# Kernel tuning notes

Hardware: AMD Instinct MI355X
Metric: run time of the kernel (lower is better)

## Reference

```python
import jax, jax.numpy as jnp
import numpy as np

B, S, H, D = 2, 2048, 16, 128
HID = H * D
THETA = 10000.0
SCALE = 1.0 / np.sqrt(D)


def setup_inputs() -> dict:
    key = jax.random.key(0)
    k1, k2, k3 = jax.random.split(key, 3)
    x = jax.random.normal(k1, (B, S, HID), dtype=jnp.float32)
    w_qkv = jax.random.normal(k2, (3 * HID, HID), dtype=jnp.float32) * 0.02
    w_o = jax.random.normal(k3, (HID, HID), dtype=jnp.float32) * 0.02
    return {"x": x, "w_qkv": w_qkv, "w_o": w_o}


def _rope_cos_sin(seq_len, dim, dtype):
    inv_freq = 1.0 / (THETA ** (jnp.arange(0, dim, 2, dtype=jnp.float32) / dim))
    pos = jnp.arange(seq_len, dtype=jnp.float32)
    freqs = pos[:, None] * inv_freq[None, :]          # (S, D/2)
    emb = jnp.concatenate([freqs, freqs], axis=-1)    # (S, D)
    return jnp.cos(emb).astype(dtype), jnp.sin(emb).astype(dtype)


def _rotate_half(t):
    t1, t2 = jnp.split(t, 2, axis=-1)
    return jnp.concatenate([-t2, t1], axis=-1)


def reference(x, w_qkv, w_o):
    b, s, _ = x.shape
    qkv = jnp.einsum('bsh,oh->bso', x, w_qkv)                 # (B,S,3*HID)
    qkv = qkv.reshape(b, s, 3, H, D).transpose(2, 0, 3, 1, 4)  # (3,B,H,S,D)
    q, k, v = qkv[0], qkv[1], qkv[2]
    cos, sin = _rope_cos_sin(s, D, x.dtype)                    # (S,D)
    q = q * cos + _rotate_half(q) * sin
    k = k * cos + _rotate_half(k) * sin
    scores = jnp.einsum('bhqd,bhkd->bhqk', q, k) * SCALE       # (B,H,S,S)
    causal = jnp.triu(jnp.ones((s, s), dtype=bool), k=1)
    scores = jnp.where(causal[None, None], -jnp.inf, scores)
    attn = jax.nn.softmax(scores.astype(jnp.float32), axis=-1).astype(q.dtype)
    out = jnp.einsum('bhqk,bhkd->bhqd', attn, v)               # (B,H,S,D)
    out = out.transpose(0, 2, 1, 3).reshape(b, s, HID)
    return jnp.einsum('bsh,oh->bso', out, w_o)
```

## Files before the change

kernel.cpp:

```cpp
#include <hip/hip_runtime.h>
#include <hip/hip_bf16.h>

typedef unsigned short u16;
typedef unsigned long long u64;
typedef u16 us8 __attribute__((ext_vector_type(8)));
typedef __bf16 bf8_t __attribute__((ext_vector_type(8)));
typedef float f32x4 __attribute__((ext_vector_type(4)));

__device__ __forceinline__ float b2f(u16 u) {
    return __uint_as_float(((unsigned int)u) << 16);
}
__device__ __forceinline__ u16 f2b(float f) {
    union { __hip_bfloat16 h; u16 u; } v;
    v.h = __float2bfloat16(f);
    return v.u;
}
__device__ __forceinline__ f32x4 mfma16(bf8_t a, bf8_t b, f32x4 c) {
    return __builtin_amdgcn_mfma_f32_16x16x32_bf16(a, b, c, 0, 0, 0);
}
__device__ __forceinline__ void gload_lds16(const u16* g, u16* lds_base) {
    __builtin_amdgcn_global_load_lds((const __attribute__((address_space(1))) unsigned int*)g,
                                     (__attribute__((address_space(3))) unsigned int*)lds_base,
                                     16, 0, 0);
}

__global__ __launch_bounds__(256) void f32_to_bf16(const float* __restrict__ src,
                                                   u16* __restrict__ dst, int n8) {
    int idx = blockIdx.x * 256 + threadIdx.x;
    if (idx >= n8) return;
    float4 f0 = ((const float4*)src)[idx * 2];
    float4 f1 = ((const float4*)src)[idx * 2 + 1];
    us8 o;
    o[0] = f2b(f0.x); o[1] = f2b(f0.y); o[2] = f2b(f0.z); o[3] = f2b(f0.w);
    o[4] = f2b(f1.x); o[5] = f2b(f1.y); o[6] = f2b(f1.z); o[7] = f2b(f1.w);
    ((us8*)dst)[idx] = o;
}

#define BARX() __builtin_amdgcn_s_barrier()
#define LGKM0() do { asm volatile("s_waitcnt lgkmcnt(0)" ::: "memory"); \
                     __builtin_amdgcn_sched_barrier(0); } while (0)
#define VM4()   do { asm volatile("s_waitcnt vmcnt(4)" ::: "memory"); \
                     __builtin_amdgcn_sched_barrier(0); } while (0)

template<int SF32>
__global__ __launch_bounds__(512, 2) void gemm256(const u16* __restrict__ A,
                                                  const u16* __restrict__ B,
                                                  void* __restrict__ Cout, int ldc) {
    __shared__ u16 LA[2][256 * 64];
    __shared__ u16 LB[2][256 * 64];

    const int tid = threadIdx.x;
    const int w = tid >> 6, lane = tid & 63;
    const int lm = lane & 15, lq = lane >> 4;
    const int wm = w >> 2, wn = w & 3;

    const int bid = blockIdx.x;
    const int nper = gridDim.x >> 3;
    const int wg = (bid & 7) * nper + (bid >> 3);
    const int mt = wg & 15, nt = wg >> 4;
    const int m0 = mt * 256, n0 = nt * 256;

    const int lp = lane ^ ((lane & 32) >> 4);
    const int srow = lp >> 3;
    const int scol = (lp & 7) * 8;

    const u16* Ag = A + (size_t)(m0 + srow) * 2048 + scol;
    const u16* Bg = B + (size_t)(n0 + srow) * 2048 + scol;

#define STAGE_A(c, h, kt) do { \
    _Pragma("unroll") \
    for (int i = 0; i < 2; i++) { \
        int R = w * 2 + i; \
        gload_lds16(Ag + (size_t)((h) * 128 + R * 8) * 2048 + (kt) * 64, \
                    &LA[c][((h) * 128 + R * 8) * 64]); \
    } } while (0)

#define STAGE_B(c, h, kt) do { \
    _Pragma("unroll") \
    for (int i = 0; i < 2; i++) { \
        int R = w * 2 + i; \
        gload_lds16(Bg + (size_t)((h) * 128 + R * 8) * 2048 + (kt) * 64, \
                    &LB[c][((h) * 128 + R * 8) * 64]); \
    } } while (0)

    bf8_t af[8][2], bfr[4][2];
    f32x4 acc[8][4] = {};

#define RD_A(c, mh) do { \
    _Pragma("unroll") \
    for (int m = 0; m < 4; m++) \
    _Pragma("unroll") \
    for (int ks = 0; ks < 2; ks++) { \
        int o = (wm * 128 + ((mh) * 4 + m) * 16 + lm) * 128 + ks * 64 + lq * 16; \
        o ^= ((o >> 9) & 1) << 5; \
        af[(mh) * 4 + m][ks] = *(const bf8_t*)((const char*)&LA[c][0] + o); \
    } } while (0)

#define RD_B(c, nh) do { \
    _Pragma("unroll") \
    for (int n = 0; n < 2; n++) \
    _Pragma("unroll") \
    for (int ks = 0; ks < 2; ks++) { \
        int o = (wn * 64 + ((nh) * 2 + n) * 16 + lm) * 128 + ks * 64 + lq * 16; \
        o ^= ((o >> 9) & 1) << 5; \
        bfr[(nh) * 2 + n][ks] = *(const bf8_t*)((const char*)&LB[c][0] + o); \
    } } while (0)

#define QUAD(mh, nh) do { \
    __builtin_amdgcn_s_setprio(1); \
    _Pragma("unroll") \
    for (int m = 0; m < 4; m++) \
    _Pragma("unroll") \
    for (int n = 0; n < 2; n++) \
    _Pragma("unroll") \
    for (int ks = 0; ks < 2; ks++) \
        acc[(mh) * 4 + m][(nh) * 2 + n] = mfma16(af[(mh) * 4 + m][ks], \
            bfr[(nh) * 2 + n][ks], acc[(mh) * 4 + m][(nh) * 2 + n]); \
    __builtin_amdgcn_s_setprio(0); \
    } while (0)

#define TILE(c, tB, tA) do { \
    RD_A(c, 0); RD_B(c, 0); \
    STAGE_B((c) ^ 1, 0, tB); \
    BARX(); LGKM0(); \
    QUAD(0, 0); \
    BARX(); \
    RD_A(c, 1); \
    STAGE_B((c) ^ 1, 1, tB); \
    BARX(); LGKM0(); \
    QUAD(1, 0); \
    BARX(); \
    RD_B(c, 1); \
    STAGE_A(c, 0, tA); \
    BARX(); LGKM0(); \
    QUAD(0, 1); \
    BARX(); \
    STAGE_A(c, 1, tA); \
    QUAD(1, 1); \
    VM4(); \
    BARX(); \
} while (0)

    STAGE_A(0, 0, 0); STAGE_A(0, 1, 0);
    STAGE_B(0, 0, 0); STAGE_B(0, 1, 0);
    STAGE_A(1, 0, 1); STAGE_A(1, 1, 1);
    VM4();
    BARX();

    for (int it = 0; it < 16; it++) {
        const int t0 = 2 * it, t1 = 2 * it + 1;
        const int tB0 = t1;
        const int tA0 = (t0 + 2 < 32) ? t0 + 2 : 31;
        const int tB1 = (t1 + 1 < 32) ? t1 + 1 : 31;
        const int tA1 = (t1 + 2 < 32) ? t1 + 2 : 31;
        TILE(0, tB0, tA0);
        TILE(1, tB1, tA1);
    }

#pragma unroll
    for (int m = 0; m < 8; m++)
#pragma unroll
        for (int n = 0; n < 4; n++)
#pragma unroll
            for (int r = 0; r < 4; r++) {
                int row = m0 + wm * 128 + m * 16 + lq * 4 + r;
                int col = n0 + wn * 64 + n * 16 + lm;
                if (SF32)
                    ((float*)Cout)[(size_t)row * ldc + col] = acc[m][n][r];
                else
                    ((u16*)Cout)[(size_t)row * ldc + col] = f2b(acc[m][n][r]);
            }
#undef TILE
#undef QUAD
#undef RD_A
#undef RD_B
#undef STAGE_A
#undef STAGE_B
}

__global__ __launch_bounds__(256) void rope_vt(u16* __restrict__ qkv, u16* __restrict__ VT) {
    __shared__ u16 T[64 * 136];
    const int tid = threadIdx.x;
    const int s0 = blockIdx.x * 64;
    const int bh = blockIdx.y;
    const int b = bh >> 4, h = bh & 15;
#pragma unroll
    for (int p = 0; p < 4; p++) {
        int sl = p * 16 + (tid >> 4);
        int d0 = (tid & 15) * 8;
        *(us8*)&T[sl * 136 + d0] =
            *(const us8*)(qkv + ((size_t)(b * 2048 + s0 + sl)) * 6144 + 4096 + h * 128 + d0);
    }
#pragma unroll
    for (int p = 0; p < 2; p++) {
        int task = p * 256 + tid;
        int sl = task >> 3;
        int jg = task & 7;
        size_t base = ((size_t)(b * 2048 + s0 + sl)) * 6144 + h * 128 + jg * 8;
        us8 qlo = *(const us8*)(qkv + base);
        us8 qhi = *(const us8*)(qkv + base + 64);
        us8 klo = *(const us8*)(qkv + base + 2048);
        us8 khi = *(const us8*)(qkv + base + 2048 + 64);
        us8 oql, oqh, okl, okh;
        float s = (float)(s0 + sl);
#pragma unroll
        for (int e = 0; e < 8; e++) {
            int j = jg * 8 + e;
            float inv = __expf((float)j * (-9.210340371976184f / 64.f));
            float ang = s * inv;
            float sn, c;
            __sincosf(ang, &sn, &c);
            float q1 = b2f(qlo[e]), q2 = b2f(qhi[e]);
            oql[e] = f2b(q1 * c - q2 * sn);
            oqh[e] = f2b(q2 * c + q1 * sn);
            float k1 = b2f(klo[e]), k2 = b2f(khi[e]);
            okl[e] = f2b(k1 * c - k2 * sn);
            okh[e] = f2b(k2 * c + k1 * sn);
        }
        *(us8*)(qkv + base) = oql;
        *(us8*)(qkv + base + 64) = oqh;
        *(us8*)(qkv + base + 2048) = okl;
        *(us8*)(qkv + base + 2048 + 64) = okh;
    }
    __syncthreads();
#pragma unroll
    for (int p = 0; p < 4; p++) {
        int idx = p * 256 + tid;
        int d = idx & 127;
        int sg = idx >> 7;
        us8 v;
#pragma unroll
        for (int i = 0; i < 8; i++) v[i] = T[(sg * 8 + i) * 136 + d];
        *(us8*)&VT[((size_t)bh * 128 + d) * 2048 + s0 + sg * 8] = v;
    }
}

#define ATT_SCALE 0.08838834764831845f

__global__ __launch_bounds__(256, 2) void attn_flash(const u16* __restrict__ qkv, const u16* __restrict__ VT,
                                                     u16* __restrict__ AO) {
    const int bid = blockIdx.x;
    const int swz = (bid & 7) * 64 + (bid >> 3);
    const int bh = swz >> 4;
    const int pair = swz & 15;
    const int b = bh >> 4, h = bh & 15;
    const int tid = threadIdx.x, lane = tid & 63, wave = tid >> 6;
    const int lm = lane & 15, lq = lane >> 4;

    const int jq0 = 31 - pair;
    const int jq1 = pair;
    const int ktmax = jq0;

    __shared__ u16 Kt[64 * 136];
    __shared__ u16 Vt[128 * 72];

    bf8_t qf[2][4];
#pragma unroll
    for (int qg = 0; qg < 2; qg++) {
        const int jqv = qg ? jq1 : jq0;
        const u16* Qrow = qkv + ((size_t)(b * 2048 + jqv * 64 + wave * 16 + lm)) * 6144 + h * 128;
#pragma unroll
        for (int ks = 0; ks < 4; ks++)
            qf[qg][ks] = *(const bf8_t*)(Qrow + ks * 32 + lq * 8);
    }

    f32x4 Of[2][8] = {};
    float mrun[2] = {-3.0e38f, -3.0e38f}, lrun[2] = {0.f, 0.f};

    const u16* Kbase = qkv + (size_t)b * 2048 * 6144 + 2048 + h * 128;
    const u16* VTbase = VT + (size_t)bh * 128 * 2048;

    const int krow = tid >> 4;
    const int kcol = (tid & 15) * 8;
    const int vrow = tid >> 3;
    const int vcol = (tid & 7) * 8;

    us8 kreg[4], vreg[4];
#pragma unroll
    for (int p = 0; p < 4; p++) {
        kreg[p] = *(const us8*)(Kbase + (size_t)(p * 16 + krow) * 6144 + kcol);
        vreg[p] = *(const us8*)(VTbase + (size_t)(p * 32 + vrow) * 2048 + vcol);
    }

    for (int kt = 0; kt <= ktmax; kt++) {
        __syncthreads();
#pragma unroll
        for (int p = 0; p < 4; p++) {
            *(us8*)&Kt[(p * 16 + krow) * 136 + kcol] = kreg[p];
            *(us8*)&Vt[(p * 32 + vrow) * 72 + vcol] = vreg[p];
        }
        __syncthreads();
        {
            int kn = (kt + 1 <= ktmax ? kt + 1 : ktmax) * 64;
#pragma unroll
            for (int p = 0; p < 4; p++) {
                kreg[p] = *(const us8*)(Kbase + (size_t)(kn + p * 16 + krow) * 6144 + kcol);
                vreg[p] = *(const us8*)(VTbase + (size_t)(p * 32 + vrow) * 2048 + kn + vcol);
            }
        }

        const bool act1 = (kt <= jq1);
        u64 pk[2][4];
#pragma unroll
        for (int qg = 0; qg < 2; qg++) {
            if (qg == 0 || act1) {
                const int jqv = qg ? jq1 : jq0;
                float sv[4][4];
#pragma unroll
                for (int nb = 0; nb < 4; nb++) {
                    f32x4 a = {};
#pragma unroll
                    for (int ks = 0; ks < 4; ks++) {
                        bf8_t kf = *(const bf8_t*)&Kt[(nb * 16 + lm) * 136 + ks * 32 + lq * 8];
                        a = mfma16(kf, qf[qg][ks], a);
                    }
#pragma unroll
                    for (int r = 0; r < 4; r++) sv[nb][r] = a[r] * ATT_SCALE;
                }
                if (kt == jqv) {
                    int qglob = jqv * 64 + wave * 16 + lm;
#pragma unroll
                    for (int nb = 0; nb < 4; nb++)
#pragma unroll
                        for (int r = 0; r < 4; r++)
                            if (kt * 64 + nb * 16 + lq * 4 + r > qglob) sv[nb][r] = -3.0e38f;
                }
                float mx = -3.0e38f;
#pragma unroll
                for (int nb = 0; nb < 4; nb++)
#pragma unroll
                    for (int r = 0; r < 4; r++) mx = fmaxf(mx, sv[nb][r]);
                mx = fmaxf(mx, __shfl_xor(mx, 16, 64));
                mx = fmaxf(mx, __shfl_xor(mx, 32, 64));
                float mnew = fmaxf(mrun[qg], mx);
                float a_ = __expf(mrun[qg] - mnew);
                float rs = 0.f;
#pragma unroll
                for (int nb = 0; nb < 4; nb++) {
                    float e0 = __expf(sv[nb][0] - mnew), e1 = __expf(sv[nb][1] - mnew);
                    float e2 = __expf(sv[nb][2] - mnew), e3 = __expf(sv[nb][3] - mnew);
                    rs += (e0 + e1) + (e2 + e3);
                    unsigned int lo = (unsigned int)f2b(e0) | ((unsigned int)f2b(e1) << 16);
                    unsigned int hi = (unsigned int)f2b(e2) | ((unsigned int)f2b(e3) << 16);
                    pk[qg][nb] = (u64)lo | ((u64)hi << 32);
                }
                rs += __shfl_xor(rs, 16, 64);
                rs += __shfl_xor(rs, 32, 64);
                lrun[qg] = lrun[qg] * a_ + rs;
                mrun[qg] = mnew;
#pragma unroll
                for (int db = 0; db < 8; db++)
#pragma unroll
                    for (int r = 0; r < 4; r++) Of[qg][db][r] *= a_;
            }
        }

        const int slo = ((lq & 1) * 2) * 16 + lm;
        const int shi = slo + 16;
        const bool sel = (lq >> 1) != 0;
#pragma unroll
        for (int kk = 0; kk < 2; kk++) {
            union { u64 v[2]; bf8_t f; } pf[2];
#pragma unroll
            for (int qg = 0; qg < 2; qg++) {
                if (qg == 0 || act1) {
                    u64 lo0 = __shfl(pk[qg][2 * kk + 0], slo, 64);
                    u64 lo1 = __shfl(pk[qg][2 * kk + 1], slo, 64);
                    u64 hi0 = __shfl(pk[qg][2 * kk + 0], shi, 64);
                    u64 hi1 = __shfl(pk[qg][2 * kk + 1], shi, 64);
                    pf[qg].v[0] = sel ? lo1 : lo0;
                    pf[qg].v[1] = sel ? hi1 : hi0;
                }
            }
#pragma unroll
            for (int db = 0; db < 8; db++) {
                bf8_t vf = *(const bf8_t*)&Vt[(db * 16 + lm) * 72 + kk * 32 + lq * 8];
                Of[0][db] = mfma16(vf, pf[0].f, Of[0][db]);
                if (act1) Of[1][db] = mfma16(vf, pf[1].f, Of[1][db]);
            }
        }
    }
#pragma unroll
    for (int qg = 0; qg < 2; qg++) {
        const int jqv = qg ? jq1 : jq0;
        float invl = 1.f / lrun[qg];
        size_t rowbase = (size_t)(b * 2048 + jqv * 64 + wave * 16 + lm) * 2048 + h * 128;
#pragma unroll
        for (int db = 0; db < 8; db++) {
            ushort4 o;
            o.x = f2b(Of[qg][db][0] * invl);
            o.y = f2b(Of[qg][db][1] * invl);
            o.z = f2b(Of[qg][db][2] * invl);
            o.w = f2b(Of[qg][db][3] * invl);
            *(ushort4*)(AO + rowbase + db * 16 + lq * 4) = o;
        }
    }
}

extern "C" void kernel_launch(void* const* d_in, const int* in_sizes, int n_in,
                              void* d_out, int out_size, void* d_ws, size_t ws_size,
                              hipStream_t stream) {
    const float* x     = (const float*)d_in[0];
    const float* w_qkv = (const float*)d_in[1];
    const float* w_o   = (const float*)d_in[2];
    float* out = (float*)d_out;
    u16* ws = (u16*)d_ws;

    u16* qkvb  = ws;
    u16* VT    = ws + 25165824;
    u16* AO    = ws + 33554432;
    u16* xb    = ws + 41943040;
    u16* wqkvb = ws + 50331648;
    u16* wob   = ws + 62914560;

    f32_to_bf16<<<4096, 256, 0, stream>>>(x, xb, 1048576);
    f32_to_bf16<<<6144, 256, 0, stream>>>(w_qkv, wqkvb, 1572864);
    f32_to_bf16<<<2048, 256, 0, stream>>>(w_o, wob, 524288);
    gemm256<0><<<384, 512, 0, stream>>>(xb, wqkvb, qkvb, 6144);
    rope_vt<<<dim3(32, 32), 256, 0, stream>>>(qkvb, VT);
    attn_flash<<<dim3(512), 256, 0, stream>>>(qkvb, VT, AO);
    gemm256<1><<<128, 512, 0, stream>>>(AO, wob, out, 2048);
}
```

Measured before the change: 454.2 us.

## Template GEMM on M-tile height; use 128-row tiles for output projection

Adds an AH template parameter so the GEMM can use 128x256 tiles instead of 256x256. The output projection now launches 256 workgroups instead of 128, which fills more of the CUs on the chip. The LDS swizzle also changes from a single-bit XOR to a full 8-way XOR of column chunks by row, to cut bank conflicts on fragment reads. Smaller tiles reuse each loaded operand less, and the changed swizzle now applies to the QKV GEMM as well.

```diff
diff --git a/kernel.cpp b/kernel.cpp
--- a/kernel.cpp
+++ b/kernel.cpp
@@ -39,14 +39,19 @@
 #define BARX() __builtin_amdgcn_s_barrier()
 #define LGKM0() do { asm volatile("s_waitcnt lgkmcnt(0)" ::: "memory"); \
                      __builtin_amdgcn_sched_barrier(0); } while (0)
-#define VM4()   do { asm volatile("s_waitcnt vmcnt(4)" ::: "memory"); \
-                     __builtin_amdgcn_sched_barrier(0); } while (0)
-
-template<int SF32>
+#define VMN() do { \
+    if constexpr (AH == 2) asm volatile("s_waitcnt vmcnt(4)" ::: "memory"); \
+    else                   asm volatile("s_waitcnt vmcnt(2)" ::: "memory"); \
+    __builtin_amdgcn_sched_barrier(0); } while (0)
+
+template<int SF32, int AH>
 __global__ __launch_bounds__(512, 2) void gemm256(const u16* __restrict__ A,
                                                   const u16* __restrict__ B,
                                                   void* __restrict__ Cout, int ldc) {
-    __shared__ u16 LA[2][256 * 64];
+    constexpr int MF = AH * 4;
+    constexpr int MH = AH * 2;
+
+    __shared__ u16 LA[2][AH * 128 * 64];
     __shared__ u16 LB[2][256 * 64];
 
     const int tid = threadIdx.x;
@@ -57,12 +62,12 @@
     const int bid = blockIdx.x;
     const int nper = gridDim.x >> 3;
     const int wg = (bid & 7) * nper + (bid >> 3);
-    const int mt = wg & 15, nt = wg >> 4;
-    const int m0 = mt * 256, n0 = nt * 256;
-
-    const int lp = lane ^ ((lane & 32) >> 4);
-    const int srow = lp >> 3;
-    const int scol = (lp & 7) * 8;
+    const int mt = (AH == 2) ? (wg & 15) : (wg & 31);
+    const int nt = (AH == 2) ? (wg >> 4) : (wg >> 5);
+    const int m0 = mt * (AH * 128), n0 = nt * 256;
+
+    const int srow = lane >> 3;
+    const int scol = ((lane & 7) ^ srow) * 8;
 
     const u16* Ag = A + (size_t)(m0 + srow) * 2048 + scol;
     const u16* Bg = B + (size_t)(n0 + srow) * 2048 + scol;
@@ -83,17 +88,18 @@
                     &LB[c][((h) * 128 + R * 8) * 64]); \
     } } while (0)
 
-    bf8_t af[8][2], bfr[4][2];
-    f32x4 acc[8][4] = {};
+    bf8_t af[MF][2], bfr[4][2];
+    f32x4 acc[MF][4] = {};
+    const int cswz = (lm & 7) << 4;
 
 #define RD_A(c, mh) do { \
     _Pragma("unroll") \
-    for (int m = 0; m < 4; m++) \
+    for (int m = 0; m < MH; m++) \
     _Pragma("unroll") \
     for (int ks = 0; ks < 2; ks++) { \
-        int o = (wm * 128 + ((mh) * 4 + m) * 16 + lm) * 128 + ks * 64 + lq * 16; \
-        o ^= ((o >> 9) & 1) << 5; \
-        af[(mh) * 4 + m][ks] = *(const bf8_t*)((const char*)&LA[c][0] + o); \
+        int row = wm * (AH * 64) + ((mh) * MH + m) * 16 + lm; \
+        int o = (row * 128 + ks * 64 + lq * 16) ^ cswz; \
+        af[(mh) * MH + m][ks] = *(const bf8_t*)((const char*)&LA[c][0] + o); \
     } } while (0)
 
 #define RD_B(c, nh) do { \
@@ -101,21 +107,21 @@
     for (int n = 0; n < 2; n++) \
     _Pragma("unroll") \
     for (int ks = 0; ks < 2; ks++) { \
-        int o = (wn * 64 + ((nh) * 2 + n) * 16 + lm) * 128 + ks * 64 + lq * 16; \
-        o ^= ((o >> 9) & 1) << 5; \
+        int row = wn * 64 + ((nh) * 2 + n) * 16 + lm; \
+        int o = (row * 128 + ks * 64 + lq * 16) ^ cswz; \
         bfr[(nh) * 2 + n][ks] = *(const bf8_t*)((const char*)&LB[c][0] + o); \
     } } while (0)
 
 #define QUAD(mh, nh) do { \
     __builtin_amdgcn_s_setprio(1); \
     _Pragma("unroll") \
-    for (int m = 0; m < 4; m++) \
+    for (int m = 0; m < MH; m++) \
     _Pragma("unroll") \
     for (int n = 0; n < 2; n++) \
     _Pragma("unroll") \
     for (int ks = 0; ks < 2; ks++) \
-        acc[(mh) * 4 + m][(nh) * 2 + n] = mfma16(af[(mh) * 4 + m][ks], \
-            bfr[(nh) * 2 + n][ks], acc[(mh) * 4 + m][(nh) * 2 + n]); \
+        acc[(mh) * MH + m][(nh) * 2 + n] = mfma16(af[(mh) * MH + m][ks], \
+            bfr[(nh) * 2 + n][ks], acc[(mh) * MH + m][(nh) * 2 + n]); \
     __builtin_amdgcn_s_setprio(0); \
     } while (0)
 
@@ -135,16 +141,18 @@
     BARX(); LGKM0(); \
     QUAD(0, 1); \
     BARX(); \
-    STAGE_A(c, 1, tA); \
+    if constexpr (AH == 2) STAGE_A(c, 1, tA); \
     QUAD(1, 1); \
-    VM4(); \
+    VMN(); \
     BARX(); \
 } while (0)
 
-    STAGE_A(0, 0, 0); STAGE_A(0, 1, 0);
+    STAGE_A(0, 0, 0);
+    if constexpr (AH == 2) STAGE_A(0, 1, 0);
     STAGE_B(0, 0, 0); STAGE_B(0, 1, 0);
-    STAGE_A(1, 0, 1); STAGE_A(1, 1, 1);
-    VM4();
+    STAGE_A(1, 0, 1);
+    if constexpr (AH == 2) STAGE_A(1, 1, 1);
+    VMN();
     BARX();
 
     for (int it = 0; it < 16; it++) {
@@ -158,12 +166,12 @@
     }
 
 #pragma unroll
-    for (int m = 0; m < 8; m++)
+    for (int m = 0; m < MF; m++)
 #pragma unroll
         for (int n = 0; n < 4; n++)
 #pragma unroll
             for (int r = 0; r < 4; r++) {
-                int row = m0 + wm * 128 + m * 16 + lq * 4 + r;
+                int row = m0 + wm * (AH * 64) + m * 16 + lq * 4 + r;
                 int col = n0 + wn * 64 + n * 16 + lm;
                 if (SF32)
                     ((float*)Cout)[(size_t)row * ldc + col] = acc[m][n][r];
@@ -416,8 +424,8 @@
     f32_to_bf16<<<4096, 256, 0, stream>>>(x, xb, 1048576);
     f32_to_bf16<<<6144, 256, 0, stream>>>(w_qkv, wqkvb, 1572864);
     f32_to_bf16<<<2048, 256, 0, stream>>>(w_o, wob, 524288);
-    gemm256<0><<<384, 512, 0, stream>>>(xb, wqkvb, qkvb, 6144);
+    gemm256<0, 2><<<384, 512, 0, stream>>>(xb, wqkvb, qkvb, 6144);
     rope_vt<<<dim3(32, 32), 256, 0, stream>>>(qkvb, VT);
     attn_flash<<<dim3(512), 256, 0, stream>>>(qkvb, VT, AO);
-    gemm256<1><<<128, 512, 0, stream>>>(AO, wob, out, 2048);
-}
+    gemm256<1, 1><<<256, 512, 0, stream>>>(AO, wob, out, 2048);
+}
```

New measurement: 416.1 us. -8.4%, faster.
